# Kernel optimization log

Measured on AMD Instinct MI355X. Metric: run time of the kernel, lower is better.

## Reference

```python
import jax, jax.numpy as jnp
import numpy as np

B = 20      # hard-coded self.batch_size in the torch module
L = 20      # max gts length (dp matrix is [B, 21, 21])
V = 100000  # vocab / number of topic classes


def setup_inputs() -> dict:
    key = jax.random.key(0)
    k1, k2 = jax.random.split(key)
    topic_prob = jax.random.uniform(k1, (B, L, V), dtype=jnp.float32)
    hard_label = jax.random.randint(k2, (B, L), 0, V, dtype=jnp.int32)
    return {"topic_prob": topic_prob, "hard_label": hard_label}


def _calcs_loss(topic_prob, hard_label):
    dtype = topic_prob.dtype
    mask = (hard_label >= 0).astype(dtype)                    # [B, L]
    lens = jnp.sum(mask, axis=1).astype(jnp.int32)            # [B] gts_len
    idx = jnp.clip(hard_label, 0, V - 1)                      # safe gather index

    # P[b, j, k] = topic_prob[b, j, hard_label[b, k]]  -> [B, L, L]
    idx_bjk = jnp.broadcast_to(idx[:, None, :], (B, L, L))
    P = jnp.take_along_axis(topic_prob, idx_bjk, axis=2)      # [B, L, L]

    mask_kT = mask.T                                          # [L, B]
    zero_col = jnp.zeros((B,), dtype)

    def outer(row_prev, j_inp):
        # row_prev: dp[j] row, shape [B, L+1]
        p_j, mj = j_inp                                       # p_j: [B, L], mj: [B]

        def inner(cur, k_inp):
            # cur = dp[j+1][k] (left neighbor in new row), shape [B]
            p, dp_diag, dp_up, mk = k_inp                     # each [B]
            val = p * (dp_diag + 1.0) + (1.0 - p) * jnp.maximum(cur, dp_up)
            val = jnp.where((mj * mk) > 0, val, jnp.zeros_like(val))
            return val, val

        xs = (p_j.T, row_prev[:, :L].T, row_prev[:, 1:].T, mask_kT)
        _, new_vals = jax.lax.scan(inner, zero_col, xs)       # [L, B]
        row_new = jnp.concatenate([zero_col[:, None], new_vals.T], axis=1)  # [B, L+1]
        return row_new, row_new

    row0 = jnp.zeros((B, L + 1), dtype)
    xs_outer = (jnp.swapaxes(P, 0, 1), mask.T)                # [L, B, L], [L, B]
    _, rows = jax.lax.scan(outer, row0, xs_outer)             # [L, B, L+1]

    dp = jnp.concatenate([row0[None], rows], axis=0)          # [L+1, B, L+1]
    dp = jnp.transpose(dp, (1, 0, 2))                         # [B, L+1, L+1]
    final = dp[jnp.arange(B), lens, lens]                     # dp[i][len_i][len_i]
    calcs = -jnp.log(final / lens.astype(dtype))              # [B]
    return jnp.sum(calcs) / B


def reference(topic_prob, hard_label):
    return _calcs_loss(topic_prob, hard_label)
```

## Files before the change

kernel.cpp:

```cpp
#include <hip/hip_runtime.h>
#include <math.h>


#define CB 20
#define CL 20
#define CV 100000

__global__ __launch_bounds__(256) void calcs_kernel(
    const float* __restrict__ topic_prob,
    const int*   __restrict__ hard_label,
    float*       __restrict__ out)
{
    __shared__ int   s_hl[CB * CL];
    __shared__ float s_P[CB * CL * CL];
    __shared__ float s_calc[CB];

    const int tid = threadIdx.x;

    for (int t = tid; t < CB * CL; t += blockDim.x) s_hl[t] = hard_label[t];
    __syncthreads();

    for (int t = tid; t < CB * CL * CL; t += blockDim.x) {
        int b   = t / (CL * CL);
        int rem = t - b * (CL * CL);
        int j   = rem / CL;
        int k   = rem - j * CL;
        int hl  = s_hl[b * CL + k];
        int idx = hl < 0 ? 0 : (hl > CV - 1 ? CV - 1 : hl);
        s_P[t] = topic_prob[(size_t)b * ((size_t)CL * CV) + (size_t)j * CV + (size_t)idx];
    }
    __syncthreads();

    if (tid < CB) {
        const int b = tid;

        float maskv[CL];
        int len = 0;
        #pragma unroll
        for (int k = 0; k < CL; ++k) {
            bool m = (s_hl[b * CL + k] >= 0);
            maskv[k] = m ? 1.0f : 0.0f;
            len += m ? 1 : 0;
        }

        float prev[CL + 1];
        float curr[CL + 1];
        #pragma unroll
        for (int kk = 0; kk <= CL; ++kk) prev[kk] = 0.0f;

        float final_v = 0.0f;
        const float* Pb = &s_P[b * CL * CL];

        for (int j = 0; j < CL; ++j) {
            float mj = (s_hl[b * CL + j] >= 0) ? 1.0f : 0.0f;
            float c = 0.0f;
            curr[0] = 0.0f;
            #pragma unroll
            for (int k = 0; k < CL; ++k) {
                float p   = Pb[j * CL + k];
                float val = p * (prev[k] + 1.0f) + (1.0f - p) * fmaxf(c, prev[k + 1]);
                val = (mj * maskv[k] > 0.0f) ? val : 0.0f;
                c = val;
                curr[k + 1] = val;
            }
            bool cap = (j + 1 == len);
            #pragma unroll
            for (int kk = 0; kk <= CL; ++kk) {
                if (cap && kk == len) final_v = curr[kk];
                prev[kk] = curr[kk];
            }
        }

        s_calc[b] = -logf(final_v / (float)len);
    }
    __syncthreads();

    if (tid == 0) {
        float s = 0.0f;
        #pragma unroll
        for (int b = 0; b < CB; ++b) s += s_calc[b];
        out[0] = s / (float)CB;
    }
}

extern "C" void kernel_launch(void* const* d_in, const int* in_sizes, int n_in,
                              void* d_out, int out_size, void* d_ws, size_t ws_size,
                              hipStream_t stream) {
    const float* topic_prob = (const float*)d_in[0];
    const int*   hard_label = (const int*)d_in[1];
    float*       out        = (float*)d_out;
    calcs_kernel<<<1, 256, 0, stream>>>(topic_prob, hard_label, out);
}
```

Measured before the change: 213.7 us.

## Batch gathers across 1024 threads and streamline DP with bitmask and shuffle reduce

Grows the block from 256 to 1024 threads and has each thread issue all of its scattered gathers into registers before writing them to shared memory. This raises the number of global loads in flight and cuts the serial latency of the 8000-element gather. The DP now updates the previous row in place, keeps the mask as a bitmask counted with popc, and replaces the shared-memory final sum with a wavefront shuffle reduction, which removes one barrier. The single-block launch still leaves most of the GPU idle.

```diff
diff --git a/kernel.cpp b/kernel.cpp
--- a/kernel.cpp
+++ b/kernel.cpp
@@ -5,46 +5,54 @@
 #define CB 20
 #define CL 20
 #define CV 100000
+#define NT 1024
+#define NP (CB * CL * CL)
+#define PER ((NP + NT - 1) / NT)
 
-__global__ __launch_bounds__(256) void calcs_kernel(
+__global__ __launch_bounds__(NT) void calcs_kernel(
     const float* __restrict__ topic_prob,
     const int*   __restrict__ hard_label,
     float*       __restrict__ out)
 {
     __shared__ int   s_hl[CB * CL];
-    __shared__ float s_P[CB * CL * CL];
-    __shared__ float s_calc[CB];
+    __shared__ float s_P[NP];
 
     const int tid = threadIdx.x;
 
-    for (int t = tid; t < CB * CL; t += blockDim.x) s_hl[t] = hard_label[t];
+    if (tid < CB * CL) s_hl[tid] = hard_label[tid];
     __syncthreads();
 
-    for (int t = tid; t < CB * CL * CL; t += blockDim.x) {
-        int b   = t / (CL * CL);
-        int rem = t - b * (CL * CL);
+    float vals[PER];
+    #pragma unroll
+    for (int i = 0; i < PER; ++i) {
+        int t  = tid + i * NT;
+        int tt = t < NP ? t : 0;
+        int b   = tt / (CL * CL);
+        int rem = tt - b * (CL * CL);
         int j   = rem / CL;
         int k   = rem - j * CL;
         int hl  = s_hl[b * CL + k];
-        int idx = hl < 0 ? 0 : (hl > CV - 1 ? CV - 1 : hl);
-        s_P[t] = topic_prob[(size_t)b * ((size_t)CL * CV) + (size_t)j * CV + (size_t)idx];
+        int ci  = hl < 0 ? 0 : (hl > CV - 1 ? CV - 1 : hl);
+        vals[i] = topic_prob[(size_t)(b * CL + j) * CV + (size_t)ci];
+    }
+    #pragma unroll
+    for (int i = 0; i < PER; ++i) {
+        int t = tid + i * NT;
+        if (t < NP) s_P[t] = vals[i];
     }
     __syncthreads();
 
+    float loss = 0.0f;
     if (tid < CB) {
         const int b = tid;
 
-        float maskv[CL];
-        int len = 0;
+        unsigned mbits = 0;
         #pragma unroll
-        for (int k = 0; k < CL; ++k) {
-            bool m = (s_hl[b * CL + k] >= 0);
-            maskv[k] = m ? 1.0f : 0.0f;
-            len += m ? 1 : 0;
-        }
+        for (int k = 0; k < CL; ++k)
+            mbits |= (s_hl[b * CL + k] >= 0 ? 1u : 0u) << k;
+        const int len = __popc(mbits);
 
         float prev[CL + 1];
-        float curr[CL + 1];
         #pragma unroll
         for (int kk = 0; kk <= CL; ++kk) prev[kk] = 0.0f;
 
@@ -52,34 +60,32 @@
         const float* Pb = &s_P[b * CL * CL];
 
         for (int j = 0; j < CL; ++j) {
-            float mj = (s_hl[b * CL + j] >= 0) ? 1.0f : 0.0f;
+            const bool mj = (mbits >> j) & 1u;
             float c = 0.0f;
-            curr[0] = 0.0f;
+            float d = prev[0];
+            float row_end = 0.0f;
             #pragma unroll
             for (int k = 0; k < CL; ++k) {
-                float p   = Pb[j * CL + k];
-                float val = p * (prev[k] + 1.0f) + (1.0f - p) * fmaxf(c, prev[k + 1]);
-                val = (mj * maskv[k] > 0.0f) ? val : 0.0f;
+                float p = Pb[j * CL + k];
+                float u = prev[k + 1];
+                float val = p * (d + 1.0f) + (1.0f - p) * fmaxf(c, u);
+                bool mk = (mbits >> k) & 1u;
+                val = (mj && mk) ? val : 0.0f;
+                d = u;
+                prev[k + 1] = val;
                 c = val;
-                curr[k + 1] = val;
+                if (k + 1 == len) row_end = val;
             }
-            bool cap = (j + 1 == len);
-            #pragma unroll
-            for (int kk = 0; kk <= CL; ++kk) {
-                if (cap && kk == len) final_v = curr[kk];
-                prev[kk] = curr[kk];
-            }
+            if (j + 1 == len) final_v = row_end;
         }
+        loss = -logf(final_v / (float)len);
+    }
 
-        s_calc[b] = -logf(final_v / (float)len);
-    }
-    __syncthreads();
-
-    if (tid == 0) {
-        float s = 0.0f;
+    if (tid < 64) {
         #pragma unroll
-        for (int b = 0; b < CB; ++b) s += s_calc[b];
-        out[0] = s / (float)CB;
+        for (int off = 32; off > 0; off >>= 1)
+            loss += __shfl_down(loss, off, 64);
+        if (tid == 0) out[0] = loss / (float)CB;
     }
 }
 
@@ -89,5 +95,5 @@
     const float* topic_prob = (const float*)d_in[0];
     const int*   hard_label = (const int*)d_in[1];
     float*       out        = (float*)d_out;
-    calcs_kernel<<<1, 256, 0, stream>>>(topic_prob, hard_label, out);
+    calcs_kernel<<<1, NT, 0, stream>>>(topic_prob, hard_label, out);
 }
```

Result: no change. 212.9 us (-0.4%).
